# Kernel optimization log

Measured on AMD Instinct MI355X. Metric: run time of the kernel, lower is better.

Reference implementation:

```python
import jax, jax.numpy as jnp
import numpy as np

DIM = 192
HEADS = 6
HEAD_DIM = DIM // HEADS
WS = 8            # window size
N = WS * WS       # tokens per window
IN_CC = 16        # top-k kept keys per query
B, H, W = 8, 64, 64
NEG = -100.0      # value used by the torch code for masked logits
EPS_NORM = 1e-12  # F.normalize eps
EPS_LN = 1e-5     # nn.LayerNorm eps


def _rel_pos_index(ws):
    coords = np.stack(np.meshgrid(np.arange(ws), np.arange(ws), indexing='ij'))  # (2,ws,ws)
    cf = coords.reshape(2, -1)
    rel = (cf[:, :, None] - cf[:, None, :]).transpose(1, 2, 0).astype(np.int64)  # (N,N,2)
    rel[:, :, 0] += ws - 1
    rel[:, :, 1] += ws - 1
    rel[:, :, 0] *= 2 * ws - 1
    return jnp.asarray(rel.sum(-1))  # (N,N) indices into (2ws-1)^2 table

REL_IDX = _rel_pos_index(WS)


def _layer_norm(x, g, b):
    mu = jnp.mean(x, -1, keepdims=True)
    var = jnp.mean(jnp.square(x - mu), -1, keepdims=True)
    return (x - mu) * jax.lax.rsqrt(var + EPS_LN) * g + b


def _l2n(x):
    n = jnp.sqrt(jnp.sum(jnp.square(x), -1, keepdims=True))
    return x / jnp.maximum(n, EPS_NORM)


def setup_inputs() -> dict:
    key = jax.random.key(0)
    ks = jax.random.split(key, 8)
    s = 0.02
    return {
        'x': jax.random.normal(ks[0], (B, DIM, H, W), jnp.float32),
        'norm1_g': jnp.ones((DIM,), jnp.float32),
        'norm1_b': jnp.zeros((DIM,), jnp.float32),
        'qkv_w': jax.random.normal(ks[1], (3 * DIM, DIM), jnp.float32) * s,
        'qkv_b': jnp.zeros((3 * DIM,), jnp.float32),
        'proj_w': jax.random.normal(ks[2], (DIM, DIM), jnp.float32) * s,
        'proj_b': jnp.zeros((DIM,), jnp.float32),
        'rpb_table': jax.random.normal(ks[3], ((2 * WS - 1) ** 2, HEADS), jnp.float32) * s,
        'temperature': jnp.ones((HEADS, 1, 1), jnp.float32),
        'norm2_g': jnp.ones((DIM,), jnp.float32),
        'norm2_b': jnp.zeros((DIM,), jnp.float32),
        'fc1_w': jax.random.normal(ks[4], (4 * DIM, DIM), jnp.float32) * s,
        'fc1_b': jnp.zeros((4 * DIM,), jnp.float32),
        'fc2_w': jax.random.normal(ks[5], (DIM, 4 * DIM), jnp.float32) * s,
        'fc2_b': jnp.zeros((DIM,), jnp.float32),
    }


def reference(x, norm1_g, norm1_b, qkv_w, qkv_b, proj_w, proj_b, rpb_table,
              temperature, norm2_g, norm2_b, fc1_w, fc1_b, fc2_w, fc2_b):
    b, c, h, w = x.shape
    # (B,C,H,W) -> (B,L,C), pre-norm (note: the torch code norms the shortcut too)
    xs = jnp.transpose(x.reshape(b, c, h * w), (0, 2, 1))
    shortcut = _layer_norm(xs, norm1_g, norm1_b)  # (B,L,C)

    # window partition: (B,H,W,C) -> (B*nWh*nWw, N, C); shift_size=0, no padding (H,W % WS == 0)
    xin = shortcut.reshape(b, h // WS, WS, w // WS, WS, c)
    xin = jnp.transpose(xin, (0, 1, 3, 2, 4, 5)).reshape(-1, N, c)
    B_ = xin.shape[0]

    qkv = (xin @ qkv_w.T + qkv_b).reshape(B_, N, 3, HEADS, HEAD_DIM)
    qkv = jnp.transpose(qkv, (2, 0, 3, 1, 4))  # (3, B_, h, N, d)
    q, k, v = qkv[0], qkv[1], qkv[2]

    # cosine attention with learned per-head temperature
    attn = jnp.einsum('bhnd,bhmd->bhnm', _l2n(q), _l2n(k)) * temperature  # (B_,h,N,N)

    # top-k sparsification: keep IN_CC largest logits per query (threshold == kth value;
    # equivalent to the torch topk+scatter mask for distinct values)
    kth = jax.lax.top_k(attn, IN_CC)[0][..., -1:]
    attn = jnp.where(attn >= kth, attn, NEG)

    # relative position bias gather: (N,N,h) -> (h,N,N)
    rpb = jnp.transpose(rpb_table[REL_IDX], (2, 0, 1))
    attn = jax.nn.softmax(attn + rpb[None], axis=-1)

    out = jnp.einsum('bhnm,bhmd->bhnd', attn, v)
    out = jnp.transpose(out, (0, 2, 1, 3)).reshape(B_, N, c)
    out = out @ proj_w.T + proj_b

    # window reverse -> (B, L, C)
    out = out.reshape(b, h // WS, w // WS, WS, WS, c)
    out = jnp.transpose(out, (0, 1, 3, 2, 4, 5)).reshape(b, h * w, c)

    x2 = shortcut + out  # drop_path = identity (eval)
    hdn = _layer_norm(x2, norm2_g, norm2_b)
    hdn = jax.nn.gelu(hdn @ fc1_w.T + fc1_b, approximate=False) @ fc2_w.T + fc2_b
    x2 = x2 + hdn

    # back to (B,C,H,W)
    return jnp.transpose(x2, (0, 2, 1)).reshape(b, c, h, w)
```

## Files before the change

kernel.cpp:

```cpp
#include <hip/hip_runtime.h>
#include <hip/hip_bf16.h>
#include <math.h>

#define DIM     192
#define HEADS   6
#define HEAD_DIM 32
#define NTOK    64
#define IN_CC   16
#define TTOT    32768
#define NWIN    512

using bf16x8 = __attribute__((ext_vector_type(8))) short;
using f32x4  = __attribute__((ext_vector_type(4))) float;
typedef unsigned short ushort_t;

__device__ __forceinline__ ushort_t f2b(float f) {
    unsigned u = __float_as_uint(f);
    u += 0x7fffu + ((u >> 16) & 1u);
    return (ushort_t)(u >> 16);
}
__device__ __forceinline__ unsigned pk2(float a, float b) {
    return (unsigned)f2b(a) | ((unsigned)f2b(b) << 16);
}
__device__ __forceinline__ float b2f(ushort_t u) {
    return __uint_as_float(((unsigned)u) << 16);
}

__global__ __launch_bounds__(256) void cvt_all_kernel(
    const float* __restrict__ s0, const float* __restrict__ s1,
    const float* __restrict__ s2, const float* __restrict__ s3,
    ushort_t* __restrict__ d0, ushort_t* __restrict__ d1,
    ushort_t* __restrict__ d2, ushort_t* __restrict__ d3)
{
    const int bid = blockIdx.x;
    const float* src; ushort_t* dst; int off, K; bool perm = false;
    if (bid < 108)      { src = s0; dst = d0; off = bid;       K = 192; perm = true; }
    else if (bid < 144) { src = s1; dst = d1; off = bid - 108; K = 192; }
    else if (bid < 288) { src = s2; dst = d2; off = bid - 144; K = 192; }
    else                { src = s3; dst = d3; off = bid - 288; K = 768; }
    const int K8 = K >> 3;
    const int d  = (off * 256 + threadIdx.x) * 4;
    const int frag = d >> 7, win = d & 127;
    const int m16w = win >> 3, k7 = win & 7;
    const int oblk = frag / K8, kblk = frag - oblk * K8;
    const int o = oblk * 16 + m16w, k = kblk * 8 + k7;
    int so = o;
    if (perm && o < 384) {
        const int s = o & 31;
        const int c = (((s >> 2) & 3) << 3) | (((s >> 4) & 1) << 2) | (s & 3);
        so = (o & ~31) | c;
    }
    float4 v = *(const float4*)(src + (size_t)so * K + k);
    ushort4 ov;
    ov.x = f2b(v.x); ov.y = f2b(v.y); ov.z = f2b(v.z); ov.w = f2b(v.w);
    *(ushort4*)(dst + d) = ov;
}

__global__ __launch_bounds__(256) void ln1_kernel(
    const float* __restrict__ x, const float* __restrict__ g,
    const float* __restrict__ bb, ushort_t* __restrict__ outh)
{
    __shared__ float xs[64][193];
    __shared__ float mu_s[64], rs_s[64];
    __shared__ float gs[192], bs[192];
    const int tid = threadIdx.x;
    const int t0  = blockIdx.x * 64;
    const int b   = t0 >> 12;
    const int hw0 = t0 & 4095;
    if (tid < 192) { gs[tid] = g[tid]; bs[tid] = bb[tid]; }
    const int tok = tid & 63, qq = tid >> 6;
    const float* xb = x + (size_t)b * (DIM * 4096) + hw0 + tok;
    #pragma unroll
    for (int it = 0; it < 48; ++it) {
        int c = it * 4 + qq;
        xs[tok][c] = xb[(size_t)c * 4096];
    }
    __syncthreads();
    const int tok2 = tid >> 2, p = tid & 3;
    float sum = 0.f;
    #pragma unroll
    for (int c = 0; c < 48; ++c) sum += xs[tok2][p * 48 + c];
    sum += __shfl_xor(sum, 1);
    sum += __shfl_xor(sum, 2);
    const float m = sum * (1.0f / 192.0f);
    float ss = 0.f;
    #pragma unroll
    for (int c = 0; c < 48; ++c) { float d = xs[tok2][p * 48 + c] - m; ss += d * d; }
    ss += __shfl_xor(ss, 1);
    ss += __shfl_xor(ss, 2);
    if (p == 0) {
        mu_s[tok2] = m;
        rs_s[tok2] = 1.0f / sqrtf(ss * (1.0f / 192.0f) + 1e-5f);
    }
    __syncthreads();
    ushort_t* obh = outh + (size_t)t0 * DIM;
    #pragma unroll
    for (int it = 0; it < 48; ++it) {
        int idx = it * 256 + tid;
        int tk = idx / 192, c = idx % 192;
        obh[idx] = f2b((xs[tk][c] - mu_s[tk]) * rs_s[tk] * gs[c] + bs[c]);
    }
}

__global__ __launch_bounds__(768, 3) void attn_fused(
    const ushort_t* __restrict__ sc_h, const ushort_t* __restrict__ wqf,
    const float* __restrict__ qkv_b, const float* __restrict__ rpb_table,
    const float* __restrict__ temp, const ushort_t* __restrict__ wpf,
    const float* __restrict__ proj_b, float* __restrict__ x2)
{
    __shared__ __align__(16) char smem[127680];
    const int tid  = threadIdx.x;
    const int wave = tid >> 6, n = tid & 63;
    char* arena = smem + wave * 9728;
    float*    Ssq = (float*)arena;
    ushort_t* Ph  = (ushort_t*)arena;
    ushort_t* Vt  = (ushort_t*)(arena + 4608);
    float*    ksb = (float*)(arena + 9216);
    float*    qnb = (float*)(arena + 9472);
    float*    rpb = (float*)(smem + 116736) + wave * 228;

    const int wloc = (wave >= 6) ? 1 : 0;
    const int h    = wave - 6 * wloc;
    ushort_t (*AoT)[200] = (ushort_t(*)[200])(smem + wloc * 25600);
    float* Cwi = (float*)(smem + 51200 + wave * 2304);

    const int win = blockIdx.x * 2 + wloc;
    const int b   = win >> 6;
    const int wh  = (win >> 3) & 7, ww = win & 7;
    const int i1  = n >> 3, j1 = n & 7;
    const int m16 = n & 15, quad = n >> 4;

    for (int r = n; r < 225; r += 64) rpb[r] = rpb_table[r * 6 + h];

    int trow[4];
    #pragma unroll
    for (int i = 0; i < 4; ++i) {
        const int row = 16 * i + m16;
        trow[i] = b * 4096 + (wh * 8 + (row >> 3)) * 64 + ww * 8 + (row & 7);
    }

    bf16x8 qA[4], kB[4];
    #pragma unroll
    for (int part = 0; part < 3; ++part) {
        const int o0 = part * 192 + h * 32;
        f32x4 pa[4][2];
        #pragma unroll
        for (int i = 0; i < 4; ++i)
            #pragma unroll
            for (int j = 0; j < 2; ++j)
                pa[i][j] = (f32x4)(0.0f);
        const ushort_t* Wb = wqf + (size_t)(o0 >> 4) * 24 * 128 + m16 * 8;
        for (int ks = 0; ks < 192; ks += 32) {
            bf16x8 af[4], wv[2];
            #pragma unroll
            for (int i = 0; i < 4; ++i)
                af[i] = *(const bf16x8*)(sc_h + (size_t)trow[i] * 192 + ks + quad * 8);
            #pragma unroll
            for (int j = 0; j < 2; ++j)
                wv[j] = *(const bf16x8*)(Wb + (size_t)(j * 24 + (ks >> 3) + quad) * 128);
            #pragma unroll
            for (int i = 0; i < 4; ++i)
                #pragma unroll
                for (int j = 0; j < 2; ++j)
                    pa[i][j] = __builtin_amdgcn_mfma_f32_16x16x32_bf16(wv[j], af[i], pa[i][j], 0, 0, 0);
        }
        if (part < 2) {
            const float4 bv0 = *(const float4*)&qkv_b[o0 + 8 * quad];
            const float4 bv1 = *(const float4*)&qkv_b[o0 + 8 * quad + 4];
            float ssq[4];
            #pragma unroll
            for (int i = 0; i < 4; ++i) {
                f32x4 v0 = pa[i][0], v1 = pa[i][1];
                v0[0] += bv0.x; v0[1] += bv0.y; v0[2] += bv0.z; v0[3] += bv0.w;
                v1[0] += bv1.x; v1[1] += bv1.y; v1[2] += bv1.z; v1[3] += bv1.w;
                float sq = 0.f;
                #pragma unroll
                for (int r = 0; r < 4; ++r) sq += v0[r] * v0[r] + v1[r] * v1[r];
                ssq[i] = sq;
                bf16x8 fr;
                fr[0] = (short)f2b(v0[0]); fr[1] = (short)f2b(v0[1]);
                fr[2] = (short)f2b(v0[2]); fr[3] = (short)f2b(v0[3]);
                fr[4] = (short)f2b(v1[0]); fr[5] = (short)f2b(v1[1]);
                fr[6] = (short)f2b(v1[2]); fr[7] = (short)f2b(v1[3]);
                if (part == 0) qA[i] = fr; else kB[i] = fr;
            }
            #pragma unroll
            for (int i = 0; i < 4; ++i) {
                ssq[i] += __shfl_xor(ssq[i], 16);
                ssq[i] += __shfl_xor(ssq[i], 32);
            }
            if (quad == 0) {
                #pragma unroll
                for (int i = 0; i < 4; ++i) {
                    if (part == 0) qnb[16 * i + m16] = ssq[i];
                    else           ksb[4 * m16 + i]  = 1.0f / fmaxf(sqrtf(ssq[i]), 1e-12f);
                }
            }
        } else {
            const float4 bv0 = *(const float4*)&qkv_b[o0 + quad * 4];
            const float4 bv1 = *(const float4*)&qkv_b[o0 + 16 + quad * 4];
            #pragma unroll
            for (int i = 0; i < 4; ++i) {
                f32x4 v0 = pa[i][0], v1 = pa[i][1];
                v0[0] += bv0.x; v0[1] += bv0.y; v0[2] += bv0.z; v0[3] += bv0.w;
                v1[0] += bv1.x; v1[1] += bv1.y; v1[2] += bv1.z; v1[3] += bv1.w;
                #pragma unroll
                for (int r = 0; r < 4; ++r) {
                    Vt[(quad * 4 + r) * 72 + 4 * m16 + i]      = f2b(v0[r]);
                    Vt[(16 + quad * 4 + r) * 72 + 4 * m16 + i] = f2b(v1[r]);
                }
            }
        }
    }

    f32x4 acc[4][4];
    #pragma unroll
    for (int i = 0; i < 4; ++i)
        #pragma unroll
        for (int j = 0; j < 4; ++j)
            acc[i][j] = __builtin_amdgcn_mfma_f32_16x16x32_bf16(qA[i], kB[j], (f32x4)(0.0f), 0, 0, 0);

    float s[64];
    #pragma unroll
    for (int i = 0; i < 4; ++i) {
        #pragma unroll
        for (int r = 0; r < 4; ++r) {
            f32x4 vv = { acc[i][0][r], acc[i][1][r], acc[i][2][r], acc[i][3][r] };
            *(f32x4*)&Ssq[(4 * quad + r) * 68 + 4 * m16] = vv;
        }
        if ((n >> 4) == i) {
            #pragma unroll
            for (int c = 0; c < 16; ++c)
                *(float4*)&s[4 * c] = *(const float4*)&Ssq[(n & 15) * 68 + 4 * c];
        }
    }

    const float qs = temp[h] / fmaxf(sqrtf(qnb[n]), 1e-12f);
    #pragma unroll
    for (int c = 0; c < 16; ++c) {
        float4 kv = *(const float4*)&ksb[4 * c];
        s[4*c+0] *= qs * kv.x; s[4*c+1] *= qs * kv.y;
        s[4*c+2] *= qs * kv.z; s[4*c+3] *= qs * kv.w;
    }

    float thr = 1e30f;
    for (int it = 0; it < IN_CC; ++it) {
        float mx = -1e30f;
        #pragma unroll
        for (int m = 0; m < 64; ++m) {
            float vv = (s[m] < thr) ? s[m] : -1e30f;
            mx = fmaxf(mx, vv);
        }
        thr = mx;
    }

    const int basen = i1 * 15 + j1;
    float mx = -1e30f;
    #pragma unroll
    for (int c = 0; c < 64; ++c) {
        const int m = 16 * (c & 3) + (c >> 2);
        const int i2 = m >> 3, j2 = m & 7;
        float vv = ((s[c] >= thr) ? s[c] : -100.0f)
                 + rpb[basen + (7 - i2) * 15 + (7 - j2)];
        s[c] = vv;
        mx = fmaxf(mx, vv);
    }
    float sum = 0.f;
    #pragma unroll
    for (int c = 0; c < 64; ++c) { float e = __expf(s[c] - mx); s[c] = e; sum += e; }
    const float inv = 1.0f / sum;
    #pragma unroll
    for (int c = 0; c < 64; ++c) s[c] *= inv;

    bf16x8 vb[2][2];
    #pragma unroll
    for (int kh2 = 0; kh2 < 2; ++kh2)
        #pragma unroll
        for (int j2 = 0; j2 < 2; ++j2)
            vb[kh2][j2] = *(const bf16x8*)&Vt[(16 * j2 + m16) * 72 + kh2 * 32 + quad * 8];

    f32x4 o[4][2];
    #pragma unroll
    for (int i = 0; i < 4; ++i)
        #pragma unroll
        for (int j2 = 0; j2 < 2; ++j2)
            o[i][j2] = (f32x4)(0.0f);
    #pragma unroll
    for (int hf = 0; hf < 2; ++hf) {
        if ((n >> 5) == hf) {
            #pragma unroll
            for (int g = 0; g < 8; ++g) {
                uint4 w;
                w.x = pk2(s[8*g+0], s[8*g+1]); w.y = pk2(s[8*g+2], s[8*g+3]);
                w.z = pk2(s[8*g+4], s[8*g+5]); w.w = pk2(s[8*g+6], s[8*g+7]);
                *(uint4*)&Ph[(n & 31) * 72 + 8 * g] = w;
            }
        }
        #pragma unroll
        for (int ih = 0; ih < 2; ++ih) {
            const int i = 2 * hf + ih;
            #pragma unroll
            for (int kh2 = 0; kh2 < 2; ++kh2) {
                bf16x8 pafr = *(const bf16x8*)&Ph[(16 * ih + m16) * 72 + kh2 * 32 + quad * 8];
                o[i][0] = __builtin_amdgcn_mfma_f32_16x16x32_bf16(pafr, vb[kh2][0], o[i][0], 0, 0, 0);
                o[i][1] = __builtin_amdgcn_mfma_f32_16x16x32_bf16(pafr, vb[kh2][1], o[i][1], 0, 0, 0);
            }
        }
    }
    __syncthreads();

    #pragma unroll
    for (int i = 0; i < 4; ++i) {
        #pragma unroll
        for (int r = 0; r < 4; ++r) {
            const int row = 16 * i + 4 * quad + r;
            AoT[row][h * 32 + m16]      = f2b(o[i][0][r]);
            AoT[row][h * 32 + 16 + m16] = f2b(o[i][1][r]);
        }
    }
    __syncthreads();

    f32x4 pacc[4][2];
    #pragma unroll
    for (int i = 0; i < 4; ++i)
        #pragma unroll
        for (int j = 0; j < 2; ++j)
            pacc[i][j] = (f32x4)(0.0f);
    const ushort_t* Wb = wpf + (size_t)(h * 2) * 24 * 128 + m16 * 8;
    for (int ks = 0; ks < 192; ks += 32) {
        bf16x8 af[4], wv[2];
        #pragma unroll
        for (int i = 0; i < 4; ++i)
            af[i] = *(const bf16x8*)&AoT[16 * i + m16][quad * 8 + ks];
        #pragma unroll
        for (int j = 0; j < 2; ++j)
            wv[j] = *(const bf16x8*)(Wb + (size_t)(j * 24 + (ks >> 3) + quad) * 128);
        #pragma unroll
        for (int i = 0; i < 4; ++i)
            #pragma unroll
            for (int j = 0; j < 2; ++j)
                pacc[i][j] = __builtin_amdgcn_mfma_f32_16x16x32_bf16(wv[j], af[i], pacc[i][j], 0, 0, 0);
    }

    const float4 bj0 = *(const float4*)&proj_b[h * 32 + quad * 4];
    const float4 bj1 = *(const float4*)&proj_b[h * 32 + 16 + quad * 4];
    const int rr = n >> 2, ccc = n & 3;
    #pragma unroll
    for (int i = 0; i < 4; ++i) {
        f32x4 v0 = pacc[i][0], v1 = pacc[i][1];
        v0[0] += bj0.x; v0[1] += bj0.y; v0[2] += bj0.z; v0[3] += bj0.w;
        v1[0] += bj1.x; v1[1] += bj1.y; v1[2] += bj1.z; v1[3] += bj1.w;
        *(f32x4*)&Cwi[m16 * 36 + quad * 4]      = v0;
        *(f32x4*)&Cwi[m16 * 36 + 16 + quad * 4] = v1;
        const int tok = 16 * i + rr;
        const int ii = tok >> 3, jj = tok & 7;
        const int tt = b * 4096 + (wh * 8 + ii) * 64 + ww * 8 + jj;
        const int oc = h * 32 + ccc * 8;
        float4 w0 = *(const float4*)&Cwi[rr * 36 + ccc * 8];
        float4 w1 = *(const float4*)&Cwi[rr * 36 + ccc * 8 + 4];
        uint4 rv = *(const uint4*)&sc_h[(size_t)tt * 192 + oc];
        w0.x += b2f((ushort_t)(rv.x & 0xffffu)); w0.y += b2f((ushort_t)(rv.x >> 16));
        w0.z += b2f((ushort_t)(rv.y & 0xffffu)); w0.w += b2f((ushort_t)(rv.y >> 16));
        w1.x += b2f((ushort_t)(rv.z & 0xffffu)); w1.y += b2f((ushort_t)(rv.z >> 16));
        w1.z += b2f((ushort_t)(rv.w & 0xffffu)); w1.w += b2f((ushort_t)(rv.w >> 16));
        *(float4*)&x2[(size_t)tt * DIM + oc]     = w0;
        *(float4*)&x2[(size_t)tt * DIM + oc + 4] = w1;
    }
}

__global__ __launch_bounds__(256) void mlp_fused(
    const float* __restrict__ x2, const ushort_t* __restrict__ w1f,
    const ushort_t* __restrict__ w2f, const float* __restrict__ fc1_b,
    const float* __restrict__ fc2_b, const float* __restrict__ g2,
    const float* __restrict__ b2, float* __restrict__ outp)
{
    __shared__ __align__(16) char smem[43008];
    ushort_t (*h_h)[200] = (ushort_t(*)[200])smem;
    ushort_t (*a1c)[136] = (ushort_t(*)[136])(smem + 25600);
    float* gs  = (float*)(smem + 25600);
    float* bs  = gs + 192;

    const int tid  = threadIdx.x;
    const int wave = tid >> 6, lane = tid & 63;
    const int m16 = lane & 15, quad = lane >> 4;
    const int t0 = blockIdx.x * 64;
    const int b   = t0 >> 12;
    const int hw0 = t0 & 4095;

    if (tid < 192) { gs[tid] = g2[tid]; bs[tid] = b2[tid]; }
    __syncthreads();
    {
        const int tok = tid >> 2, p = tid & 3;
        const float* rp = x2 + (size_t)(t0 + tok) * DIM + p * 48;
        float xv[48];
        #pragma unroll
        for (int c4 = 0; c4 < 12; ++c4)
            *(float4*)&xv[c4 * 4] = *(const float4*)(rp + c4 * 4);
        float sum = 0.f;
        #pragma unroll
        for (int c = 0; c < 48; ++c) sum += xv[c];
        sum += __shfl_xor(sum, 1);
        sum += __shfl_xor(sum, 2);
        const float m = sum * (1.0f / 192.0f);
        float ss = 0.f;
        #pragma unroll
        for (int c = 0; c < 48; ++c) { float d = xv[c] - m; ss += d * d; }
        ss += __shfl_xor(ss, 1);
        ss += __shfl_xor(ss, 2);
        const float rs = 1.0f / sqrtf(ss * (1.0f / 192.0f) + 1e-5f);
        ushort_t* hp = &h_h[tok][p * 48];
        #pragma unroll
        for (int c2 = 0; c2 < 24; ++c2) {
            float v0 = (xv[2*c2]   - m) * rs * gs[p * 48 + 2*c2]   + bs[p * 48 + 2*c2];
            float v1 = (xv[2*c2+1] - m) * rs * gs[p * 48 + 2*c2+1] + bs[p * 48 + 2*c2+1];
            *(unsigned*)(hp + 2 * c2) = pk2(v0, v1);
        }
    }
    __syncthreads();

    f32x4 acc2[4][3];
    #pragma unroll
    for (int i = 0; i < 4; ++i)
        #pragma unroll
        for (int j = 0; j < 3; ++j)
            acc2[i][j] = (f32x4)(0.0f);

    for (int c = 0; c < 6; ++c) {
        f32x4 acc1[4][2];
        #pragma unroll
        for (int i = 0; i < 4; ++i)
            #pragma unroll
            for (int j = 0; j < 2; ++j)
                acc1[i][j] = (f32x4)(0.0f);
        const ushort_t* Wb1 = w1f + (size_t)(c * 8 + wave * 2) * 24 * 128 + m16 * 8;
        for (int ks = 0; ks < 192; ks += 32) {
            bf16x8 af[4], wv[2];
            #pragma unroll
            for (int i = 0; i < 4; ++i)
                af[i] = *(const bf16x8*)&h_h[16 * i + m16][quad * 8 + ks];
            #pragma unroll
            for (int j = 0; j < 2; ++j)
                wv[j] = *(const bf16x8*)(Wb1 + (size_t)(j * 24 + (ks >> 3) + quad) * 128);
            #pragma unroll
            for (int i = 0; i < 4; ++i)
                #pragma unroll
                for (int j = 0; j < 2; ++j)
                    acc1[i][j] = __builtin_amdgcn_mfma_f32_16x16x32_bf16(wv[j], af[i], acc1[i][j], 0, 0, 0);
        }
        #pragma unroll
        for (int j = 0; j < 2; ++j) {
            const int o = c * 128 + wave * 32 + 16 * j + quad * 4;
            const float4 bv = *(const float4*)&fc1_b[o];
            #pragma unroll
            for (int i = 0; i < 4; ++i) {
                f32x4 v = acc1[i][j];
                v[0] += bv.x; v[1] += bv.y; v[2] += bv.z; v[3] += bv.w;
                #pragma unroll
                for (int r = 0; r < 4; ++r) {
                    float xg = v[r];
                    float e1 = __expf(xg * (1.5957691f + 0.0713548f * xg * xg)) + 1.0f;
                    v[r] = xg - xg * __builtin_amdgcn_rcpf(e1);
                }
                uint2 pkd;
                pkd.x = pk2(v[0], v[1]); pkd.y = pk2(v[2], v[3]);
                *(uint2*)&a1c[16 * i + m16][wave * 32 + 16 * j + quad * 4] = pkd;
            }
        }
        __syncthreads();
        const ushort_t* Wb2 = w2f + (size_t)(wave * 3) * 96 * 128 + m16 * 8;
        for (int ks = 0; ks < 128; ks += 32) {
            bf16x8 af2[4], wv2[3];
            #pragma unroll
            for (int i = 0; i < 4; ++i)
                af2[i] = *(const bf16x8*)&a1c[16 * i + m16][quad * 8 + ks];
            #pragma unroll
            for (int j = 0; j < 3; ++j)
                wv2[j] = *(const bf16x8*)(Wb2 + (size_t)(j * 96 + c * 16 + (ks >> 3) + quad) * 128);
            #pragma unroll
            for (int i = 0; i < 4; ++i)
                #pragma unroll
                for (int j = 0; j < 3; ++j)
                    acc2[i][j] = __builtin_amdgcn_mfma_f32_16x16x32_bf16(wv2[j], af2[i], acc2[i][j], 0, 0, 0);
        }
        __syncthreads();
    }

    float (*Cw)[68] = (float(*)[68])(smem + wave * 8704);
    float4 b2j[3];
    #pragma unroll
    for (int j = 0; j < 3; ++j)
        b2j[j] = *(const float4*)&fc2_b[wave * 48 + 16 * j + quad * 4];
    #pragma unroll
    for (int p = 0; p < 2; ++p) {
        #pragma unroll
        for (int ih = 0; ih < 2; ++ih) {
            const int i = 2 * p + ih;
            #pragma unroll
            for (int j = 0; j < 3; ++j) {
                f32x4 v = acc2[i][j];
                v[0] += b2j[j].x; v[1] += b2j[j].y; v[2] += b2j[j].z; v[3] += b2j[j].w;
                *(f32x4*)&Cw[ih * 16 + m16][16 * j + quad * 4] = v;
            }
        }
        #pragma unroll
        for (int q = 0; q < 6; ++q) {
            const int idx = q * 64 + lane;
            const int cc = idx >> 3, t4 = (idx & 7) * 4;
            const int o  = wave * 48 + cc;
            const int tb = t0 + p * 32 + t4;
            float4 vv;
            vv.x = Cw[t4 + 0][cc] + x2[(size_t)(tb + 0) * DIM + o];
            vv.y = Cw[t4 + 1][cc] + x2[(size_t)(tb + 1) * DIM + o];
            vv.z = Cw[t4 + 2][cc] + x2[(size_t)(tb + 2) * DIM + o];
            vv.w = Cw[t4 + 3][cc] + x2[(size_t)(tb + 3) * DIM + o];
            *(float4*)&outp[(size_t)b * (DIM * 4096) + (size_t)o * 4096
                            + hw0 + p * 32 + t4] = vv;
        }
    }
}

extern "C" void kernel_launch(void* const* d_in, const int* in_sizes, int n_in,
                              void* d_out, int out_size, void* d_ws, size_t ws_size,
                              hipStream_t stream)
{
    const float* x        = (const float*)d_in[0];
    const float* norm1_g  = (const float*)d_in[1];
    const float* norm1_b  = (const float*)d_in[2];
    const float* qkv_w    = (const float*)d_in[3];
    const float* qkv_b    = (const float*)d_in[4];
    const float* proj_w   = (const float*)d_in[5];
    const float* proj_b   = (const float*)d_in[6];
    const float* rpbt     = (const float*)d_in[7];
    const float* temp     = (const float*)d_in[8];
    const float* norm2_g  = (const float*)d_in[9];
    const float* norm2_b  = (const float*)d_in[10];
    const float* fc1_w    = (const float*)d_in[11];
    const float* fc1_b    = (const float*)d_in[12];
    const float* fc2_w    = (const float*)d_in[13];
    const float* fc2_b    = (const float*)d_in[14];
    float* out = (float*)d_out;

    char* wsb = (char*)d_ws;
    ushort_t* shortcut_h = (ushort_t*)wsb;
    float*    x2         = (float*)(wsb + 12582912);
    ushort_t* wq  = (ushort_t*)(wsb + 125829120);
    ushort_t* wp  = wq + 110592;
    ushort_t* w1  = wp + 36864;
    ushort_t* w2  = w1 + 147456;

    hipLaunchKernelGGL(cvt_all_kernel, dim3(432), dim3(256), 0, stream,
                       qkv_w, proj_w, fc1_w, fc2_w, wq, wp, w1, w2);

    hipLaunchKernelGGL(ln1_kernel, dim3(TTOT / 64), dim3(256), 0, stream,
                       x, norm1_g, norm1_b, shortcut_h);
    hipLaunchKernelGGL(attn_fused, dim3(NWIN / 2), dim3(768), 0, stream,
                       shortcut_h, wq, qkv_b, rpbt, temp, wp, proj_b, x2);
    hipLaunchKernelGGL(mlp_fused, dim3(TTOT / 64), dim3(256), 0, stream,
                       x2, w1, w2, fc1_b, fc2_b, norm2_g, norm2_b, out);
}
```

Before: 207.2 us.

## Stage window activations in LDS, fuse Q/K projections, tree-reduce top-k max

The attention kernel first copies each window's 64x192 bf16 normalized activations into shared memory cooperatively. It then computes the Q and K projections in one fused MFMA loop that reads A fragments from LDS rather than re-reading global memory once per Q/K/V part. The shared-memory layout is reorganized, the residual reads are prefetched early and the epilogue writes use a different lane mapping. The serial max chains in the top-k threshold search and softmax become 3-way tree reductions to shorten dependency chains, at the cost of more live registers and extra barriers.

```diff
diff --git a/kernel.cpp b/kernel.cpp
--- a/kernel.cpp
+++ b/kernel.cpp
@@ -24,6 +24,9 @@
 }
 __device__ __forceinline__ float b2f(ushort_t u) {
     return __uint_as_float(((unsigned)u) << 16);
+}
+__device__ __forceinline__ float m3(float a, float b, float c) {
+    return fmaxf(fmaxf(a, b), c);
 }
 
 __global__ __launch_bounds__(256) void cvt_all_kernel(
@@ -111,114 +114,164 @@
     __shared__ __align__(16) char smem[127680];
     const int tid  = threadIdx.x;
     const int wave = tid >> 6, n = tid & 63;
-    char* arena = smem + wave * 9728;
-    float*    Ssq = (float*)arena;
-    ushort_t* Ph  = (ushort_t*)arena;
-    ushort_t* Vt  = (ushort_t*)(arena + 4608);
-    float*    ksb = (float*)(arena + 9216);
-    float*    qnb = (float*)(arena + 9472);
+
+    char* Rb = smem + wave * 4608;
+    float*    Ssq = (float*)Rb;
+    ushort_t* Ph  = (ushort_t*)Rb;
+    char* Ab = smem + 55296 + wave * 5120;
+    ushort_t* Vt  = (ushort_t*)Ab;
+    float*    ksb = (float*)(Ab + 4608);
+    float*    qnb = (float*)(Ab + 4864);
     float*    rpb = (float*)(smem + 116736) + wave * 228;
 
     const int wloc = (wave >= 6) ? 1 : 0;
     const int h    = wave - 6 * wloc;
+    ushort_t* tile = (ushort_t*)(smem + wloc * 25600);
     ushort_t (*AoT)[200] = (ushort_t(*)[200])(smem + wloc * 25600);
-    float* Cwi = (float*)(smem + 51200 + wave * 2304);
+    float* Cwi = (float*)(smem + 55296 + wave * 2304);
 
     const int win = blockIdx.x * 2 + wloc;
     const int b   = win >> 6;
     const int wh  = (win >> 3) & 7, ww = win & 7;
+    const int wb  = b * 4096 + wh * 512 + ww * 8;
     const int i1  = n >> 3, j1 = n & 7;
     const int m16 = n & 15, quad = n >> 4;
 
     for (int r = n; r < 225; r += 64) rpb[r] = rpb_table[r * 6 + h];
 
-    int trow[4];
-    #pragma unroll
-    for (int i = 0; i < 4; ++i) {
-        const int row = 16 * i + m16;
-        trow[i] = b * 4096 + (wh * 8 + (row >> 3)) * 64 + ww * 8 + (row & 7);
-    }
-
+    #pragma unroll
+    for (int l = 0; l < 4; ++l) {
+        const int g = h * 256 + l * 64 + n;
+        const int t = (g * 2731) >> 16;
+        const int r = g - t * 24;
+        const int tt = wb + ((t >> 3) << 6) + (t & 7);
+        uint4 v = *(const uint4*)(sc_h + (size_t)tt * 192 + r * 8);
+        *(uint4*)(tile + t * 200 + r * 8) = v;
+    }
+    __syncthreads();
+
+    const ushort_t* tb = tile + m16 * 200 + quad * 8;
+    f32x4 pq[4][2], pk[4][2];
+    #pragma unroll
+    for (int i = 0; i < 4; ++i)
+        #pragma unroll
+        for (int j = 0; j < 2; ++j) { pq[i][j] = (f32x4)(0.0f); pk[i][j] = (f32x4)(0.0f); }
+    {
+        const ushort_t* WbQ = wqf + (size_t)(2 * h) * 3072 + m16 * 8;
+        const ushort_t* WbK = wqf + (size_t)(12 + 2 * h) * 3072 + m16 * 8;
+        for (int ks = 0; ks < 192; ks += 32) {
+            bf16x8 af[4], wq2[2], wk2[2];
+            #pragma unroll
+            for (int i = 0; i < 4; ++i)
+                af[i] = *(const bf16x8*)(tb + i * 3200 + ks);
+            #pragma unroll
+            for (int j = 0; j < 2; ++j) {
+                wq2[j] = *(const bf16x8*)(WbQ + (size_t)(j * 24 + (ks >> 3) + quad) * 128);
+                wk2[j] = *(const bf16x8*)(WbK + (size_t)(j * 24 + (ks >> 3) + quad) * 128);
+            }
+            #pragma unroll
+            for (int i = 0; i < 4; ++i)
+                #pragma unroll
+                for (int j = 0; j < 2; ++j) {
+                    pq[i][j] = __builtin_amdgcn_mfma_f32_16x16x32_bf16(wq2[j], af[i], pq[i][j], 0, 0, 0);
+                    pk[i][j] = __builtin_amdgcn_mfma_f32_16x16x32_bf16(wk2[j], af[i], pk[i][j], 0, 0, 0);
+                }
+        }
+    }
     bf16x8 qA[4], kB[4];
     #pragma unroll
-    for (int part = 0; part < 3; ++part) {
+    for (int part = 0; part < 2; ++part) {
         const int o0 = part * 192 + h * 32;
-        f32x4 pa[4][2];
+        const float4 bv0 = *(const float4*)&qkv_b[o0 + 8 * quad];
+        const float4 bv1 = *(const float4*)&qkv_b[o0 + 8 * quad + 4];
+        float ssq[4];
+        #pragma unroll
+        for (int i = 0; i < 4; ++i) {
+            f32x4 v0 = part ? pk[i][0] : pq[i][0];
+            f32x4 v1 = part ? pk[i][1] : pq[i][1];
+            v0[0] += bv0.x; v0[1] += bv0.y; v0[2] += bv0.z; v0[3] += bv0.w;
+            v1[0] += bv1.x; v1[1] += bv1.y; v1[2] += bv1.z; v1[3] += bv1.w;
+            float sq = 0.f;
+            #pragma unroll
+            for (int r = 0; r < 4; ++r) sq += v0[r] * v0[r] + v1[r] * v1[r];
+            ssq[i] = sq;
+            bf16x8 fr;
+            fr[0] = (short)f2b(v0[0]); fr[1] = (short)f2b(v0[1]);
+            fr[2] = (short)f2b(v0[2]); fr[3] = (short)f2b(v0[3]);
+            fr[4] = (short)f2b(v1[0]); fr[5] = (short)f2b(v1[1]);
+            fr[6] = (short)f2b(v1[2]); fr[7] = (short)f2b(v1[3]);
+            if (part == 0) qA[i] = fr; else kB[i] = fr;
+        }
+        #pragma unroll
+        for (int i = 0; i < 4; ++i) {
+            ssq[i] += __shfl_xor(ssq[i], 16);
+            ssq[i] += __shfl_xor(ssq[i], 32);
+        }
+        if (quad == 0) {
+            #pragma unroll
+            for (int i = 0; i < 4; ++i) {
+                if (part == 0) qnb[16 * i + m16] = ssq[i];
+                else           ksb[4 * m16 + i]  = 1.0f / fmaxf(sqrtf(ssq[i]), 1e-12f);
+            }
+        }
+    }
+
+    f32x4 acc[4][4];
+    #pragma unroll
+    for (int i = 0; i < 4; ++i)
+        #pragma unroll
+        for (int j = 0; j < 4; ++j)
+            acc[i][j] = __builtin_amdgcn_mfma_f32_16x16x32_bf16(qA[i], kB[j], (f32x4)(0.0f), 0, 0, 0);
+
+    {
+        f32x4 pv[4][2];
         #pragma unroll
         for (int i = 0; i < 4; ++i)
             #pragma unroll
+            for (int j = 0; j < 2; ++j) pv[i][j] = (f32x4)(0.0f);
+        const ushort_t* WbV = wqf + (size_t)(24 + 2 * h) * 3072 + m16 * 8;
+        for (int ks = 0; ks < 192; ks += 32) {
+            bf16x8 af[4], wv2[2];
+            #pragma unroll
+            for (int i = 0; i < 4; ++i)
+                af[i] = *(const bf16x8*)(tb + i * 3200 + ks);
+            #pragma unroll
             for (int j = 0; j < 2; ++j)
-                pa[i][j] = (f32x4)(0.0f);
-        const ushort_t* Wb = wqf + (size_t)(o0 >> 4) * 24 * 128 + m16 * 8;
-        for (int ks = 0; ks < 192; ks += 32) {
-            bf16x8 af[4], wv[2];
-            #pragma unroll
-            for (int i = 0; i < 4; ++i)
-                af[i] = *(const bf16x8*)(sc_h + (size_t)trow[i] * 192 + ks + quad * 8);
-            #pragma unroll
-            for (int j = 0; j < 2; ++j)
-                wv[j] = *(const bf16x8*)(Wb + (size_t)(j * 24 + (ks >> 3) + quad) * 128);
+                wv2[j] = *(const bf16x8*)(WbV + (size_t)(j * 24 + (ks >> 3) + quad) * 128);
             #pragma unroll
             for (int i = 0; i < 4; ++i)
                 #pragma unroll
                 for (int j = 0; j < 2; ++j)
-                    pa[i][j] = __builtin_amdgcn_mfma_f32_16x16x32_bf16(wv[j], af[i], pa[i][j], 0, 0, 0);
-        }
-        if (part < 2) {
-            const float4 bv0 = *(const float4*)&qkv_b[o0 + 8 * quad];
-            const float4 bv1 = *(const float4*)&qkv_b[o0 + 8 * quad + 4];
-            float ssq[4];
-            #pragma unroll
-            for (int i = 0; i < 4; ++i) {
-                f32x4 v0 = pa[i][0], v1 = pa[i][1];
-                v0[0] += bv0.x; v0[1] += bv0.y; v0[2] += bv0.z; v0[3] += bv0.w;
-                v1[0] += bv1.x; v1[1] += bv1.y; v1[2] += bv1.z; v1[3] += bv1.w;
-                float sq = 0.f;
-                #pragma unroll
-                for (int r = 0; r < 4; ++r) sq += v0[r] * v0[r] + v1[r] * v1[r];
-                ssq[i] = sq;
-                bf16x8 fr;
-                fr[0] = (short)f2b(v0[0]); fr[1] = (short)f2b(v0[1]);
-                fr[2] = (short)f2b(v0[2]); fr[3] = (short)f2b(v0[3]);
-                fr[4] = (short)f2b(v1[0]); fr[5] = (short)f2b(v1[1]);
-                fr[6] = (short)f2b(v1[2]); fr[7] = (short)f2b(v1[3]);
-                if (part == 0) qA[i] = fr; else kB[i] = fr;
+                    pv[i][j] = __builtin_amdgcn_mfma_f32_16x16x32_bf16(wv2[j], af[i], pv[i][j], 0, 0, 0);
+        }
+        const int o0 = 384 + h * 32;
+        const float4 bv0 = *(const float4*)&qkv_b[o0 + quad * 4];
+        const float4 bv1 = *(const float4*)&qkv_b[o0 + 16 + quad * 4];
+        #pragma unroll
+        for (int i = 0; i < 4; ++i) {
+            f32x4 v0 = pv[i][0], v1 = pv[i][1];
+            v0[0] += bv0.x; v0[1] += bv0.y; v0[2] += bv0.z; v0[3] += bv0.w;
+            v1[0] += bv1.x; v1[1] += bv1.y; v1[2] += bv1.z; v1[3] += bv1.w;
+            #pragma unroll
+            for (int r = 0; r < 4; ++r) {
+                Vt[(quad * 4 + r) * 72 + 4 * m16 + i]      = f2b(v0[r]);
+                Vt[(16 + quad * 4 + r) * 72 + 4 * m16 + i] = f2b(v1[r]);
             }
-            #pragma unroll
-            for (int i = 0; i < 4; ++i) {
-                ssq[i] += __shfl_xor(ssq[i], 16);
-                ssq[i] += __shfl_xor(ssq[i], 32);
-            }
-            if (quad == 0) {
-                #pragma unroll
-                for (int i = 0; i < 4; ++i) {
-                    if (part == 0) qnb[16 * i + m16] = ssq[i];
-                    else           ksb[4 * m16 + i]  = 1.0f / fmaxf(sqrtf(ssq[i]), 1e-12f);
-                }
-            }
-        } else {
-            const float4 bv0 = *(const float4*)&qkv_b[o0 + quad * 4];
-            const float4 bv1 = *(const float4*)&qkv_b[o0 + 16 + quad * 4];
-            #pragma unroll
-            for (int i = 0; i < 4; ++i) {
-                f32x4 v0 = pa[i][0], v1 = pa[i][1];
-                v0[0] += bv0.x; v0[1] += bv0.y; v0[2] += bv0.z; v0[3] += bv0.w;
-                v1[0] += bv1.x; v1[1] += bv1.y; v1[2] += bv1.z; v1[3] += bv1.w;
-                #pragma unroll
-                for (int r = 0; r < 4; ++r) {
-                    Vt[(quad * 4 + r) * 72 + 4 * m16 + i]      = f2b(v0[r]);
-                    Vt[(16 + quad * 4 + r) * 72 + 4 * m16 + i] = f2b(v1[r]);
-                }
-            }
-        }
-    }
-
-    f32x4 acc[4][4];
+        }
+    }
+
+    const int r8 = n >> 3, c4 = (n & 7) * 4;
+    uint2 rv[4][2];
     #pragma unroll
     for (int i = 0; i < 4; ++i)
         #pragma unroll
-        for (int j = 0; j < 4; ++j)
-            acc[i][j] = __builtin_amdgcn_mfma_f32_16x16x32_bf16(qA[i], kB[j], (f32x4)(0.0f), 0, 0, 0);
+        for (int q = 0; q < 2; ++q) {
+            const int tok = 16 * i + 8 * q + r8;
+            const int tt = wb + ((tok >> 3) << 6) + (tok & 7);
+            rv[i][q] = *(const uint2*)(sc_h + (size_t)tt * 192 + h * 32 + c4);
+        }
+
+    __syncthreads();
 
     float s[64];
     #pragma unroll
@@ -245,17 +298,21 @@
 
     float thr = 1e30f;
     for (int it = 0; it < IN_CC; ++it) {
-        float mx = -1e30f;
-        #pragma unroll
-        for (int m = 0; m < 64; ++m) {
-            float vv = (s[m] < thr) ? s[m] : -1e30f;
-            mx = fmaxf(mx, vv);
-        }
-        thr = mx;
+        #define MK(c) ((s[(c)] < thr) ? s[(c)] : -1e30f)
+        float w[22];
+        #pragma unroll
+        for (int g = 0; g < 21; ++g) w[g] = m3(MK(3*g), MK(3*g+1), MK(3*g+2));
+        w[21] = MK(63);
+        #undef MK
+        float y[8];
+        #pragma unroll
+        for (int g = 0; g < 7; ++g) y[g] = m3(w[3*g], w[3*g+1], w[3*g+2]);
+        y[7] = w[21];
+        thr = m3(m3(y[0], y[1], y[2]), m3(y[3], y[4], y[5]), fmaxf(y[6], y[7]));
     }
 
     const int basen = i1 * 15 + j1;
-    float mx = -1e30f;
+    float mxp[8];
     #pragma unroll
     for (int c = 0; c < 64; ++c) {
         const int m = 16 * (c & 3) + (c >> 2);
@@ -263,8 +320,10 @@
         float vv = ((s[c] >= thr) ? s[c] : -100.0f)
                  + rpb[basen + (7 - i2) * 15 + (7 - j2)];
         s[c] = vv;
-        mx = fmaxf(mx, vv);
-    }
+        if (c < 8) mxp[c] = vv; else mxp[c & 7] = fmaxf(mxp[c & 7], vv);
+    }
+    const float mx = m3(m3(mxp[0], mxp[1], mxp[2]), m3(mxp[3], mxp[4], mxp[5]),
+                        fmaxf(mxp[6], mxp[7]));
     float sum = 0.f;
     #pragma unroll
     for (int c = 0; c < 64; ++c) { float e = __expf(s[c] - mx); s[c] = e; sum += e; }
@@ -344,7 +403,6 @@
 
     const float4 bj0 = *(const float4*)&proj_b[h * 32 + quad * 4];
     const float4 bj1 = *(const float4*)&proj_b[h * 32 + 16 + quad * 4];
-    const int rr = n >> 2, ccc = n & 3;
     #pragma unroll
     for (int i = 0; i < 4; ++i) {
         f32x4 v0 = pacc[i][0], v1 = pacc[i][1];
@@ -352,19 +410,19 @@
         v1[0] += bj1.x; v1[1] += bj1.y; v1[2] += bj1.z; v1[3] += bj1.w;
         *(f32x4*)&Cwi[m16 * 36 + quad * 4]      = v0;
         *(f32x4*)&Cwi[m16 * 36 + 16 + quad * 4] = v1;
-        const int tok = 16 * i + rr;
-        const int ii = tok >> 3, jj = tok & 7;
-        const int tt = b * 4096 + (wh * 8 + ii) * 64 + ww * 8 + jj;
-        const int oc = h * 32 + ccc * 8;
-        float4 w0 = *(const float4*)&Cwi[rr * 36 + ccc * 8];
-        float4 w1 = *(const float4*)&Cwi[rr * 36 + ccc * 8 + 4];
-        uint4 rv = *(const uint4*)&sc_h[(size_t)tt * 192 + oc];
-        w0.x += b2f((ushort_t)(rv.x & 0xffffu)); w0.y += b2f((ushort_t)(rv.x >> 16));
-        w0.z += b2f((ushort_t)(rv.y & 0xffffu)); w0.w += b2f((ushort_t)(rv.y >> 16));
-        w1.x += b2f((ushort_t)(rv.z & 0xffffu)); w1.y += b2f((ushort_t)(rv.z >> 16));
-        w1.z += b2f((ushort_t)(rv.w & 0xffffu)); w1.w += b2f((ushort_t)(rv.w >> 16));
-        *(float4*)&x2[(size_t)tt * DIM + oc]     = w0;
-        *(float4*)&x2[(size_t)tt * DIM + oc + 4] = w1;
+        #pragma unroll
+        for (int q = 0; q < 2; ++q) {
+            const int row = 8 * q + r8;
+            const int tok = 16 * i + row;
+            const int tt = wb + ((tok >> 3) << 6) + (tok & 7);
+            float4 vv = *(const float4*)&Cwi[row * 36 + c4];
+            const uint2 rr = rv[i][q];
+            vv.x += b2f((ushort_t)(rr.x & 0xffffu));
+            vv.y += b2f((ushort_t)(rr.x >> 16));
+            vv.z += b2f((ushort_t)(rr.y & 0xffffu));
+            vv.w += b2f((ushort_t)(rr.y >> 16));
+            *(float4*)&x2[(size_t)tt * DIM + h * 32 + c4] = vv;
+        }
     }
 }
 
```

Measured after the change: 194.0 us. 6.4% less time.
